# Optimization experiments

Measured on AMD Instinct MI355X. Metric: run time of the kernel, lower is better.

## Reference

```python
import jax, jax.numpy as jnp
import numpy as np

NUM_ROUTES = 1152
NUM_CAPS = 10
IN_CH = 8
OUT_CH = 16
NUM_ITERS = 3
BATCH = 256


def squash(s, axis=-1, eps=1e-9):
    # standard capsule squash over the capsule-vector (out_channels) axis
    sq_norm = jnp.sum(s * s, axis=axis, keepdims=True)
    return (sq_norm / (1.0 + sq_norm)) * (s / jnp.sqrt(sq_norm + eps))


def setup_inputs() -> dict:
    key = jax.random.key(0)
    kx, kw = jax.random.split(key)
    x = jax.random.normal(kx, (BATCH, NUM_ROUTES, IN_CH), dtype=jnp.float32)
    # kaiming_uniform-ish init: bound = sqrt(6 / fan_in), fan_in = in_channels
    bound = float(np.sqrt(6.0 / IN_CH))
    W = jax.random.uniform(kw, (1, NUM_ROUTES, NUM_CAPS, OUT_CH, IN_CH),
                           dtype=jnp.float32, minval=-bound, maxval=bound)
    return {"x": x, "W": W}


def reference(x, W):
    # x: [B, R, I]; W: [1, R, C, O, I]
    B = x.shape[0]
    Wr = W[0]  # [R, C, O, I]
    # u_hat = W @ x  -> [B, R, C, O] (equivalent to matmul with x unsqueezed)
    u_hat = jnp.einsum('rcoi,bri->brco', Wr, x)

    b_ij = jnp.zeros((NUM_ROUTES, NUM_CAPS), dtype=x.dtype)  # shared over batch
    v_j = None
    c_ij = None
    for it in range(NUM_ITERS):
        c_ij = jax.nn.softmax(b_ij, axis=0)                 # softmax over routes
        s_j = jnp.einsum('rc,brco->bco', c_ij, u_hat)       # [B, C, O]
        v_j = squash(s_j, axis=-1)
        if it < NUM_ITERS - 1:
            # agreement: u_hat^T v, averaged over batch
            a_ij = jnp.einsum('brco,bco->brc', u_hat, v_j)  # [B, R, C]
            b_ij = b_ij + jnp.mean(a_ij, axis=0)

    # match torch output shapes: v_j.squeeze(1) -> [B, C, O, 1]; c_ij -> [B, R, C, 1, 1]
    v_out = v_j[..., None]
    c_out = jnp.broadcast_to(c_ij[None, :, :, None, None],
                             (B, NUM_ROUTES, NUM_CAPS, 1, 1))
    return v_out, c_out
```

## Files before the change

kernel.cpp:

```cpp
#include <hip/hip_runtime.h>
#include <math.h>


typedef __attribute__((ext_vector_type(8))) short short8v;
typedef __attribute__((ext_vector_type(4))) float f32x4;

__device__ __forceinline__ unsigned short f2bf(float f) {
    unsigned u = __float_as_uint(f);
    u += 0x7FFFu + ((u >> 16) & 1u);
    return (unsigned short)(u >> 16);
}
__device__ __forceinline__ float bf2f(unsigned short h) {
    return __uint_as_float(((unsigned)h) << 16);
}

union ShMem {
    struct { alignas(16) short Bs[2][12][80][8]; float cl[120]; } g;
    struct { short Th[16][256]; short Tl[16][256]; } t;
};

__global__ __launch_bounds__(256) void k_sM(const float* __restrict__ x,
                                            const float* __restrict__ W,
                                            const float* __restrict__ cw,
                                            float* __restrict__ s_part,
                                            unsigned short* __restrict__ xTh,
                                            unsigned short* __restrict__ xTl,
                                            const float* __restrict__ bcsrc,
                                            float* __restrict__ out,
                                            int tail)
{
    __shared__ ShMem sh;
    const int bid = blockIdx.x;
    const int tid = threadIdx.x;

    if (bid >= 768) {
        if (tail == 1) {
            const int m0 = (bid - 768) * 16;
            const int b = tid;
#pragma unroll
            for (int q = 0; q < 4; ++q) {
                const float4 v = reinterpret_cast<const float4*>(x)[(size_t)b * 2304 + (m0 >> 2) + q];
                const unsigned short h0 = f2bf(v.x), h1 = f2bf(v.y), h2 = f2bf(v.z), h3 = f2bf(v.w);
                sh.t.Th[q * 4 + 0][b] = (short)h0;
                sh.t.Th[q * 4 + 1][b] = (short)h1;
                sh.t.Th[q * 4 + 2][b] = (short)h2;
                sh.t.Th[q * 4 + 3][b] = (short)h3;
                sh.t.Tl[q * 4 + 0][b] = (short)f2bf(v.x - bf2f(h0));
                sh.t.Tl[q * 4 + 1][b] = (short)f2bf(v.y - bf2f(h1));
                sh.t.Tl[q * 4 + 2][b] = (short)f2bf(v.z - bf2f(h2));
                sh.t.Tl[q * 4 + 3][b] = (short)f2bf(v.w - bf2f(h3));
            }
            __syncthreads();
            const int m = tid >> 4, seg = tid & 15;
            const size_t o = (size_t)(m0 + m) * 256 + seg * 16;
            *reinterpret_cast<uint4*>(xTh + o) = *reinterpret_cast<const uint4*>(&sh.t.Th[m][seg * 16]);
            *reinterpret_cast<uint4*>(xTh + o + 8) = *reinterpret_cast<const uint4*>(&sh.t.Th[m][seg * 16 + 8]);
            *reinterpret_cast<uint4*>(xTl + o) = *reinterpret_cast<const uint4*>(&sh.t.Tl[m][seg * 16]);
            *reinterpret_cast<uint4*>(xTl + o + 8) = *reinterpret_cast<const uint4*>(&sh.t.Tl[m][seg * 16 + 8]);
        } else {
            const int i = (bid - 768) * 256 + tid;
            const float4 v = reinterpret_cast<const float4*>(bcsrc)[i % 2880];
            reinterpret_cast<float4*>(out + 40960)[i] = v;
        }
        return;
    }

    const int xcd  = bid & 7;
    const int j    = bid >> 3;
    const int kb   = (j % 12) * 8 + xcd;
    const int mtnt = j / 12;
    const int mt = mtnt >> 1;
    const int nt = mtnt & 1;
    const int w    = tid >> 6;
    const int lane = tid & 63;
    const int l15  = lane & 15;
    const int lqw  = lane >> 4;
    const int row  = mt * 64 + w * 16 + l15;
    const int n0   = nt * 80;
    const int r_base = kb * 12;

    float4 af[3][2];
    const float* xrow = x + (size_t)row * 9216 + kb * 96 + lqw * 8;
#pragma unroll
    for (int ks = 0; ks < 3; ++ks) {
        af[ks][0] = *reinterpret_cast<const float4*>(xrow + ks * 32);
        af[ks][1] = *reinterpret_cast<const float4*>(xrow + ks * 32 + 4);
    }

    if (tid < 120) sh.g.cl[tid] = cw ? cw[r_base * 10 + tid] : (1.0f / 1152.0f);
    __syncthreads();

    for (int idx = tid; idx < 960; idx += 256) {
        const int n = idx / 12, ch = idx % 12;
        const int gn = n0 + n;
        const int c = gn >> 4, o = gn & 15;
        const float sc = sh.g.cl[ch * 10 + c];
        const float* wp = &W[(size_t)(r_base + ch) * 1280 + c * 128 + o * 8];
        const float4 w0 = *reinterpret_cast<const float4*>(wp);
        const float4 w1 = *reinterpret_cast<const float4*>(wp + 4);
        float v[8] = { w0.x * sc, w0.y * sc, w0.z * sc, w0.w * sc,
                       w1.x * sc, w1.y * sc, w1.z * sc, w1.w * sc };
        short8v hv, lv;
#pragma unroll
        for (int q = 0; q < 8; ++q) {
            const unsigned short h = f2bf(v[q]);
            hv[q] = (short)h;
            lv[q] = (short)f2bf(v[q] - bf2f(h));
        }
        *reinterpret_cast<short8v*>(&sh.g.Bs[0][ch][n][0]) = hv;
        *reinterpret_cast<short8v*>(&sh.g.Bs[1][ch][n][0]) = lv;
    }

    short8v ah[3], al[3];
#pragma unroll
    for (int ks = 0; ks < 3; ++ks) {
        const float* av = reinterpret_cast<const float*>(&af[ks][0]);
#pragma unroll
        for (int q = 0; q < 8; ++q) {
            const unsigned short h = f2bf(av[q]);
            ah[ks][q] = (short)h;
            al[ks][q] = (short)f2bf(av[q] - bf2f(h));
        }
    }
    __syncthreads();

    f32x4 acc[5];
#pragma unroll
    for (int t = 0; t < 5; ++t) acc[t] = (f32x4){0.f, 0.f, 0.f, 0.f};

#pragma unroll
    for (int ks = 0; ks < 3; ++ks) {
        const int ch = ks * 4 + lqw;
#pragma unroll
        for (int t = 0; t < 5; ++t) {
            const short8v bh = *reinterpret_cast<const short8v*>(&sh.g.Bs[0][ch][t * 16 + l15][0]);
            const short8v bl = *reinterpret_cast<const short8v*>(&sh.g.Bs[1][ch][t * 16 + l15][0]);
            acc[t] = __builtin_amdgcn_mfma_f32_16x16x32_bf16(ah[ks], bh, acc[t], 0, 0, 0);
            acc[t] = __builtin_amdgcn_mfma_f32_16x16x32_bf16(ah[ks], bl, acc[t], 0, 0, 0);
            acc[t] = __builtin_amdgcn_mfma_f32_16x16x32_bf16(al[ks], bh, acc[t], 0, 0, 0);
        }
    }

    const int crow0 = mt * 64 + w * 16 + lqw * 4;
#pragma unroll
    for (int t = 0; t < 5; ++t) {
#pragma unroll
        for (int v = 0; v < 4; ++v) {
            s_part[((size_t)kb * 256 + crow0 + v) * 160 + n0 + t * 16 + l15] = acc[t][v];
        }
    }
}

__global__ __launch_bounds__(192) void k_rvT(const float* __restrict__ s_part,
                                             unsigned short* __restrict__ vTh,
                                             unsigned short* __restrict__ vTl)
{
    const int b = blockIdx.x;
    const int n = threadIdx.x;
    if (n < 160) {
        const float* p = s_part + (size_t)b * 160 + n;
        float s0 = 0.f, s1 = 0.f, s2 = 0.f, s3 = 0.f, s4 = 0.f, s5 = 0.f, s6 = 0.f, s7 = 0.f;
#pragma unroll
        for (int kbv = 0; kbv < 96; kbv += 8) {
            s0 += p[(size_t)(kbv + 0) * 40960];
            s1 += p[(size_t)(kbv + 1) * 40960];
            s2 += p[(size_t)(kbv + 2) * 40960];
            s3 += p[(size_t)(kbv + 3) * 40960];
            s4 += p[(size_t)(kbv + 4) * 40960];
            s5 += p[(size_t)(kbv + 5) * 40960];
            s6 += p[(size_t)(kbv + 6) * 40960];
            s7 += p[(size_t)(kbv + 7) * 40960];
        }
        const float s = ((s0 + s1) + (s2 + s3)) + ((s4 + s5) + (s6 + s7));
        float sq = s * s;
#pragma unroll
        for (int off = 1; off < 16; off <<= 1) sq += __shfl_xor(sq, off, 16);
        const float scale = (sq / (1.f + sq)) / sqrtf(sq + 1e-9f);
        const float val = s * scale;
        const unsigned short h = f2bf(val);
        vTh[n * 256 + b] = h;
        vTl[n * 256 + b] = f2bf(val - bf2f(h));
    }
}

__global__ __launch_bounds__(128) void k_aM(const unsigned short* __restrict__ vTh,
                                            const unsigned short* __restrict__ vTl,
                                            const unsigned short* __restrict__ xTh,
                                            const unsigned short* __restrict__ xTl,
                                            const float* __restrict__ W,
                                            float* __restrict__ dbp)
{
    __shared__ float dbl[20];
    const int mt = blockIdx.x >> 1;
    const int kh = blockIdx.x & 1;
    const int m0 = mt * 16;
    const int r0 = m0 >> 3;
    const int b0 = kh * 128;
    const int tid  = threadIdx.x;
    const int w    = tid >> 6;
    const int lane = tid & 63;
    const int l15  = lane & 15;
    const int lqw  = lane >> 4;
    if (tid < 20) dbl[tid] = 0.f;

    const size_t xbase = (size_t)(m0 + l15) * 256 + b0 + lqw * 8;

    f32x4 acc[5];
#pragma unroll
    for (int t = 0; t < 5; ++t) acc[t] = (f32x4){0.f, 0.f, 0.f, 0.f};

#pragma unroll
    for (int ks = 0; ks < 4; ++ks) {
        const short8v bh = *reinterpret_cast<const short8v*>(xTh + xbase + ks * 32);
        const short8v bl = *reinterpret_cast<const short8v*>(xTl + xbase + ks * 32);
#pragma unroll
        for (int t = 0; t < 5; ++t) {
            const size_t vbase = (size_t)(w * 80 + t * 16 + l15) * 256 + b0 + lqw * 8 + ks * 32;
            const short8v ah = *reinterpret_cast<const short8v*>(vTh + vbase);
            const short8v al = *reinterpret_cast<const short8v*>(vTl + vbase);
            acc[t] = __builtin_amdgcn_mfma_f32_16x16x32_bf16(ah, bh, acc[t], 0, 0, 0);
            acc[t] = __builtin_amdgcn_mfma_f32_16x16x32_bf16(ah, bl, acc[t], 0, 0, 0);
            acc[t] = __builtin_amdgcn_mfma_f32_16x16x32_bf16(al, bh, acc[t], 0, 0, 0);
        }
    }

    __syncthreads();
    const int rloc = l15 >> 3;
    const int i = l15 & 7;
    const int r = r0 + rloc;
#pragma unroll
    for (int t = 0; t < 5; ++t) {
        const int c = w * 5 + t;
        const float* wp = &W[(((size_t)(r * 10 + c) * 16 + lqw * 4) * 8) + i];
        float pv = wp[0] * acc[t][0] + wp[8] * acc[t][1] + wp[16] * acc[t][2] + wp[24] * acc[t][3];
        pv += __shfl_xor(pv, 16);
        pv += __shfl_xor(pv, 32);
        pv += __shfl_xor(pv, 1);
        pv += __shfl_xor(pv, 2);
        pv += __shfl_xor(pv, 4);
        if ((lane & 55) == 0)
            dbl[rloc * 10 + c] = pv;
    }
    __syncthreads();
    if (tid < 20) dbp[(size_t)kh * 11520 + (r0 + tid / 10) * 10 + (tid % 10)] = dbl[tid];
}

__global__ __launch_bounds__(128) void k_sm(const float* __restrict__ bprev,
                                            const float* __restrict__ dbp,
                                            float* __restrict__ bnew,
                                            float* __restrict__ cij)
{
    __shared__ float red[2];
    __shared__ float red2[2];
    const int c = blockIdx.x;
    const int tid = threadIdx.x;
    float bv[9];
#pragma unroll
    for (int j = 0; j < 9; ++j) {
        const int idx = (tid + j * 128) * 10 + c;
        const float d = dbp[idx] + dbp[11520 + idx];
        bv[j] = (bprev ? bprev[idx] : 0.f) + d * (1.0f / 256.0f);
    }
    float mx = bv[0];
#pragma unroll
    for (int j = 1; j < 9; ++j) mx = fmaxf(mx, bv[j]);
#pragma unroll
    for (int off = 1; off < 64; off <<= 1) mx = fmaxf(mx, __shfl_xor(mx, off, 64));
    if ((tid & 63) == 0) red[tid >> 6] = mx;
    __syncthreads();
    mx = fmaxf(red[0], red[1]);
    float es[9], lsum = 0.f;
#pragma unroll
    for (int j = 0; j < 9; ++j) { es[j] = expf(bv[j] - mx); lsum += es[j]; }
#pragma unroll
    for (int off = 1; off < 64; off <<= 1) lsum += __shfl_xor(lsum, off, 64);
    if ((tid & 63) == 0) red2[tid >> 6] = lsum;
    __syncthreads();
    const float inv = 1.f / (red2[0] + red2[1]);
#pragma unroll
    for (int j = 0; j < 9; ++j) {
        const int idx = (tid + j * 128) * 10 + c;
        bnew[idx] = bv[j];
        cij[idx] = es[j] * inv;
    }
}

__global__ __launch_bounds__(256) void k_rv(const float* __restrict__ s_part,
                                            float* __restrict__ out)
{
    const int e = blockIdx.x * 256 + threadIdx.x;
    float s0 = 0.f, s1 = 0.f, s2 = 0.f, s3 = 0.f;
#pragma unroll
    for (int kbv = 0; kbv < 96; kbv += 4) {
        s0 += s_part[(size_t)(kbv + 0) * 40960 + e];
        s1 += s_part[(size_t)(kbv + 1) * 40960 + e];
        s2 += s_part[(size_t)(kbv + 2) * 40960 + e];
        s3 += s_part[(size_t)(kbv + 3) * 40960 + e];
    }
    const float s = (s0 + s1) + (s2 + s3);
    float sq = s * s;
#pragma unroll
    for (int off = 1; off < 16; off <<= 1) sq += __shfl_xor(sq, off, 16);
    const float scale = (sq / (1.f + sq)) / sqrtf(sq + 1e-9f);
    out[e] = s * scale;
}

extern "C" void kernel_launch(void* const* d_in, const int* in_sizes, int n_in,
                              void* d_out, int out_size, void* d_ws, size_t ws_size,
                              hipStream_t stream)
{
    const float* x = (const float*)d_in[0];
    const float* W = (const float*)d_in[1];
    float* out = (float*)d_out;

    unsigned short* xTh = (unsigned short*)d_ws;
    unsigned short* xTl = xTh + 2359296;
    unsigned short* vTh = xTl + 2359296;
    unsigned short* vTl = vTh + 40960;
    float* s_part = (float*)(vTl + 40960 + 32);
    float* b1   = s_part + 3932160;
    float* b2   = b1 + 11520;
    float* c2   = b2 + 11520;
    float* c3   = c2 + 11520;
    float* dbp0 = c3 + 11520;
    float* dbp1 = dbp0 + 23040;

    k_sM<<<768 + 576, 256, 0, stream>>>(x, W, nullptr, s_part,
                                        xTh, xTl, nullptr, out, 1);
    k_rvT<<<256, 192, 0, stream>>>(s_part, vTh, vTl);
    k_aM<<<1152, 128, 0, stream>>>(vTh, vTl, xTh, xTl, W, dbp0);
    k_sm<<<10, 128, 0, stream>>>(nullptr, dbp0, b1, c2);

    k_sM<<<768, 256, 0, stream>>>(x, W, c2, s_part,
                                  xTh, xTl, nullptr, out, 0);
    k_rvT<<<256, 192, 0, stream>>>(s_part, vTh, vTl);
    k_aM<<<1152, 128, 0, stream>>>(vTh, vTl, xTh, xTl, W, dbp1);
    k_sm<<<10, 128, 0, stream>>>(b1, dbp1, b2, c3);

    k_sM<<<768 + 2880, 256, 0, stream>>>(x, W, c3, s_part,
                                         xTh, xTl, c3, out, 2);
    k_rv<<<160, 256, 0, stream>>>(s_part, out);
}
```

Before: 104.9 us.

## Retile s-GEMM: 48 K-splits with two route chunks, 32-wide N tiles

Changes the k_sM GEMM decomposition. K-split blocks drop from 96 to 48, and each block now loops over two 12-route chunks. N tiles shrink from 80 to 32 columns, giving 5 N-tiles and 960 GEMM blocks. The aim is to halve the s_part partial-sum traffic and the reduction work in k_rvT and k_rv, while adding parallelism across N. In exchange, each block does serial chunk work with an extra barrier, and each block converts x for only 32 columns, so A-fragment conversion repeats across more N tiles.

```diff
diff --git a/kernel.cpp b/kernel.cpp
--- a/kernel.cpp
+++ b/kernel.cpp
@@ -15,9 +15,11 @@
 }
 
 union ShMem {
-    struct { alignas(16) short Bs[2][12][80][8]; float cl[120]; } g;
+    struct { alignas(16) short Bs[2][12][32][8]; float cl[240]; } g;
     struct { short Th[16][256]; short Tl[16][256]; } t;
 };
+
+#define GEMM_BLOCKS 960
 
 __global__ __launch_bounds__(256) void k_sM(const float* __restrict__ x,
                                             const float* __restrict__ W,
@@ -33,9 +35,9 @@
     const int bid = blockIdx.x;
     const int tid = threadIdx.x;
 
-    if (bid >= 768) {
+    if (bid >= GEMM_BLOCKS) {
         if (tail == 1) {
-            const int m0 = (bid - 768) * 16;
+            const int m0 = (bid - GEMM_BLOCKS) * 16;
             const int b = tid;
 #pragma unroll
             for (int q = 0; q < 4; ++q) {
@@ -58,7 +60,7 @@
             *reinterpret_cast<uint4*>(xTl + o) = *reinterpret_cast<const uint4*>(&sh.t.Tl[m][seg * 16]);
             *reinterpret_cast<uint4*>(xTl + o + 8) = *reinterpret_cast<const uint4*>(&sh.t.Tl[m][seg * 16 + 8]);
         } else {
-            const int i = (bid - 768) * 256 + tid;
+            const int i = (bid - GEMM_BLOCKS) * 256 + tid;
             const float4 v = reinterpret_cast<const float4*>(bcsrc)[i % 2880];
             reinterpret_cast<float4*>(out + 40960)[i] = v;
         }
@@ -67,83 +69,89 @@
 
     const int xcd  = bid & 7;
     const int j    = bid >> 3;
-    const int kb   = (j % 12) * 8 + xcd;
-    const int mtnt = j / 12;
-    const int mt = mtnt >> 1;
-    const int nt = mtnt & 1;
+    const int kb   = (j % 6) * 8 + xcd;
+    const int mtnt = j / 6;
+    const int mt = mtnt / 5;
+    const int nt = mtnt % 5;
     const int w    = tid >> 6;
     const int lane = tid & 63;
     const int l15  = lane & 15;
     const int lqw  = lane >> 4;
     const int row  = mt * 64 + w * 16 + l15;
-    const int n0   = nt * 80;
-    const int r_base = kb * 12;
-
-    float4 af[3][2];
-    const float* xrow = x + (size_t)row * 9216 + kb * 96 + lqw * 8;
-#pragma unroll
-    for (int ks = 0; ks < 3; ++ks) {
-        af[ks][0] = *reinterpret_cast<const float4*>(xrow + ks * 32);
-        af[ks][1] = *reinterpret_cast<const float4*>(xrow + ks * 32 + 4);
-    }
-
-    if (tid < 120) sh.g.cl[tid] = cw ? cw[r_base * 10 + tid] : (1.0f / 1152.0f);
-    __syncthreads();
-
-    for (int idx = tid; idx < 960; idx += 256) {
-        const int n = idx / 12, ch = idx % 12;
-        const int gn = n0 + n;
-        const int c = gn >> 4, o = gn & 15;
-        const float sc = sh.g.cl[ch * 10 + c];
-        const float* wp = &W[(size_t)(r_base + ch) * 1280 + c * 128 + o * 8];
-        const float4 w0 = *reinterpret_cast<const float4*>(wp);
-        const float4 w1 = *reinterpret_cast<const float4*>(wp + 4);
-        float v[8] = { w0.x * sc, w0.y * sc, w0.z * sc, w0.w * sc,
-                       w1.x * sc, w1.y * sc, w1.z * sc, w1.w * sc };
-        short8v hv, lv;
-#pragma unroll
-        for (int q = 0; q < 8; ++q) {
-            const unsigned short h = f2bf(v[q]);
-            hv[q] = (short)h;
-            lv[q] = (short)f2bf(v[q] - bf2f(h));
-        }
-        *reinterpret_cast<short8v*>(&sh.g.Bs[0][ch][n][0]) = hv;
-        *reinterpret_cast<short8v*>(&sh.g.Bs[1][ch][n][0]) = lv;
-    }
-
-    short8v ah[3], al[3];
-#pragma unroll
-    for (int ks = 0; ks < 3; ++ks) {
-        const float* av = reinterpret_cast<const float*>(&af[ks][0]);
-#pragma unroll
-        for (int q = 0; q < 8; ++q) {
-            const unsigned short h = f2bf(av[q]);
-            ah[ks][q] = (short)h;
-            al[ks][q] = (short)f2bf(av[q] - bf2f(h));
-        }
-    }
-    __syncthreads();
-
-    f32x4 acc[5];
-#pragma unroll
-    for (int t = 0; t < 5; ++t) acc[t] = (f32x4){0.f, 0.f, 0.f, 0.f};
-
-#pragma unroll
-    for (int ks = 0; ks < 3; ++ks) {
-        const int ch = ks * 4 + lqw;
-#pragma unroll
-        for (int t = 0; t < 5; ++t) {
-            const short8v bh = *reinterpret_cast<const short8v*>(&sh.g.Bs[0][ch][t * 16 + l15][0]);
-            const short8v bl = *reinterpret_cast<const short8v*>(&sh.g.Bs[1][ch][t * 16 + l15][0]);
-            acc[t] = __builtin_amdgcn_mfma_f32_16x16x32_bf16(ah[ks], bh, acc[t], 0, 0, 0);
-            acc[t] = __builtin_amdgcn_mfma_f32_16x16x32_bf16(ah[ks], bl, acc[t], 0, 0, 0);
-            acc[t] = __builtin_amdgcn_mfma_f32_16x16x32_bf16(al[ks], bh, acc[t], 0, 0, 0);
-        }
+    const int n0   = nt * 32;
+    const int r_base = kb * 24;
+
+    float4 af[2][3][2];
+    const float* xrow = x + (size_t)row * 9216 + kb * 192 + lqw * 8;
+#pragma unroll
+    for (int c = 0; c < 2; ++c)
+#pragma unroll
+        for (int ks = 0; ks < 3; ++ks) {
+            af[c][ks][0] = *reinterpret_cast<const float4*>(xrow + c * 96 + ks * 32);
+            af[c][ks][1] = *reinterpret_cast<const float4*>(xrow + c * 96 + ks * 32 + 4);
+        }
+
+    if (tid < 240) sh.g.cl[tid] = cw ? cw[r_base * 10 + tid] : (1.0f / 1152.0f);
+    __syncthreads();
+
+    f32x4 acc[2];
+#pragma unroll
+    for (int t = 0; t < 2; ++t) acc[t] = (f32x4){0.f, 0.f, 0.f, 0.f};
+
+    for (int chunk = 0; chunk < 2; ++chunk) {
+        for (int idx = tid; idx < 384; idx += 256) {
+            const int n = idx / 12, ch = idx % 12;
+            const int gn = n0 + n;
+            const int c = gn >> 4, o = gn & 15;
+            const int rr = chunk * 12 + ch;
+            const float sc = sh.g.cl[rr * 10 + c];
+            const float* wp = &W[(size_t)(r_base + rr) * 1280 + c * 128 + o * 8];
+            const float4 w0 = *reinterpret_cast<const float4*>(wp);
+            const float4 w1 = *reinterpret_cast<const float4*>(wp + 4);
+            float v[8] = { w0.x * sc, w0.y * sc, w0.z * sc, w0.w * sc,
+                           w1.x * sc, w1.y * sc, w1.z * sc, w1.w * sc };
+            short8v hv, lv;
+#pragma unroll
+            for (int q = 0; q < 8; ++q) {
+                const unsigned short h = f2bf(v[q]);
+                hv[q] = (short)h;
+                lv[q] = (short)f2bf(v[q] - bf2f(h));
+            }
+            *reinterpret_cast<short8v*>(&sh.g.Bs[0][ch][n][0]) = hv;
+            *reinterpret_cast<short8v*>(&sh.g.Bs[1][ch][n][0]) = lv;
+        }
+
+        short8v ah[3], al[3];
+#pragma unroll
+        for (int ks = 0; ks < 3; ++ks) {
+            const float* av = reinterpret_cast<const float*>(&af[chunk][ks][0]);
+#pragma unroll
+            for (int q = 0; q < 8; ++q) {
+                const unsigned short h = f2bf(av[q]);
+                ah[ks][q] = (short)h;
+                al[ks][q] = (short)f2bf(av[q] - bf2f(h));
+            }
+        }
+        __syncthreads();
+
+#pragma unroll
+        for (int ks = 0; ks < 3; ++ks) {
+            const int ch = ks * 4 + lqw;
+#pragma unroll
+            for (int t = 0; t < 2; ++t) {
+                const short8v bh = *reinterpret_cast<const short8v*>(&sh.g.Bs[0][ch][t * 16 + l15][0]);
+                const short8v bl = *reinterpret_cast<const short8v*>(&sh.g.Bs[1][ch][t * 16 + l15][0]);
+                acc[t] = __builtin_amdgcn_mfma_f32_16x16x32_bf16(ah[ks], bh, acc[t], 0, 0, 0);
+                acc[t] = __builtin_amdgcn_mfma_f32_16x16x32_bf16(ah[ks], bl, acc[t], 0, 0, 0);
+                acc[t] = __builtin_amdgcn_mfma_f32_16x16x32_bf16(al[ks], bh, acc[t], 0, 0, 0);
+            }
+        }
+        if (chunk == 0) __syncthreads();
     }
 
     const int crow0 = mt * 64 + w * 16 + lqw * 4;
 #pragma unroll
-    for (int t = 0; t < 5; ++t) {
+    for (int t = 0; t < 2; ++t) {
 #pragma unroll
         for (int v = 0; v < 4; ++v) {
             s_part[((size_t)kb * 256 + crow0 + v) * 160 + n0 + t * 16 + l15] = acc[t][v];
@@ -161,7 +169,7 @@
         const float* p = s_part + (size_t)b * 160 + n;
         float s0 = 0.f, s1 = 0.f, s2 = 0.f, s3 = 0.f, s4 = 0.f, s5 = 0.f, s6 = 0.f, s7 = 0.f;
 #pragma unroll
-        for (int kbv = 0; kbv < 96; kbv += 8) {
+        for (int kbv = 0; kbv < 48; kbv += 8) {
             s0 += p[(size_t)(kbv + 0) * 40960];
             s1 += p[(size_t)(kbv + 1) * 40960];
             s2 += p[(size_t)(kbv + 2) * 40960];
@@ -291,7 +299,7 @@
     const int e = blockIdx.x * 256 + threadIdx.x;
     float s0 = 0.f, s1 = 0.f, s2 = 0.f, s3 = 0.f;
 #pragma unroll
-    for (int kbv = 0; kbv < 96; kbv += 4) {
+    for (int kbv = 0; kbv < 48; kbv += 4) {
         s0 += s_part[(size_t)(kbv + 0) * 40960 + e];
         s1 += s_part[(size_t)(kbv + 1) * 40960 + e];
         s2 += s_part[(size_t)(kbv + 2) * 40960 + e];
@@ -318,26 +326,26 @@
     unsigned short* vTh = xTl + 2359296;
     unsigned short* vTl = vTh + 40960;
     float* s_part = (float*)(vTl + 40960 + 32);
-    float* b1   = s_part + 3932160;
+    float* b1   = s_part + 48 * 40960;
     float* b2   = b1 + 11520;
     float* c2   = b2 + 11520;
     float* c3   = c2 + 11520;
     float* dbp0 = c3 + 11520;
     float* dbp1 = dbp0 + 23040;
 
-    k_sM<<<768 + 576, 256, 0, stream>>>(x, W, nullptr, s_part,
-                                        xTh, xTl, nullptr, out, 1);
+    k_sM<<<GEMM_BLOCKS + 576, 256, 0, stream>>>(x, W, nullptr, s_part,
+                                                xTh, xTl, nullptr, out, 1);
     k_rvT<<<256, 192, 0, stream>>>(s_part, vTh, vTl);
     k_aM<<<1152, 128, 0, stream>>>(vTh, vTl, xTh, xTl, W, dbp0);
     k_sm<<<10, 128, 0, stream>>>(nullptr, dbp0, b1, c2);
 
-    k_sM<<<768, 256, 0, stream>>>(x, W, c2, s_part,
-                                  xTh, xTl, nullptr, out, 0);
+    k_sM<<<GEMM_BLOCKS, 256, 0, stream>>>(x, W, c2, s_part,
+                                          xTh, xTl, nullptr, out, 0);
     k_rvT<<<256, 192, 0, stream>>>(s_part, vTh, vTl);
     k_aM<<<1152, 128, 0, stream>>>(vTh, vTl, xTh, xTl, W, dbp1);
     k_sm<<<10, 128, 0, stream>>>(b1, dbp1, b2, c3);
 
-    k_sM<<<768 + 2880, 256, 0, stream>>>(x, W, c3, s_part,
-                                         xTh, xTl, c3, out, 2);
+    k_sM<<<GEMM_BLOCKS + 2880, 256, 0, stream>>>(x, W, c3, s_part,
+                                                 xTh, xTl, c3, out, 2);
     k_rv<<<160, 256, 0, stream>>>(s_part, out);
 }
```

Result: no change. 104.4 us (-0.4%).
